# Performance work log

Measured on AMD Instinct MI355X. Metric: run time of the kernel, lower is better.

Reference implementation:

```python
import jax, jax.numpy as jnp
import numpy as np

DIM = 1024
EPS = 1e-5

def layernorm(x, g, b):
    m = jnp.mean(x, axis=-1, keepdims=True)
    v = jnp.var(x, axis=-1, keepdims=True)
    return (x - m) / jnp.sqrt(v + EPS) * g + b

def setup_inputs() -> dict:
    key = jax.random.key(0)
    ks = jax.random.split(key, 12)
    B, L, D = 4, 2048, DIM
    s = 1.0 / np.sqrt(D)
    return {
        "q": jax.random.normal(ks[0], (B, L, D), jnp.float32),
        "k": jax.random.normal(ks[1], (B, L, D), jnp.float32),
        "v": jax.random.normal(ks[2], (B, L, D), jnp.float32),
        "gq": jnp.ones((D,), jnp.float32), "bq": jnp.zeros((D,), jnp.float32),
        "gk": jnp.ones((D,), jnp.float32), "bk": jnp.zeros((D,), jnp.float32),
        "gv": jnp.ones((D,), jnp.float32), "bv": jnp.zeros((D,), jnp.float32),
        "Wq": jax.random.uniform(ks[3], (D, D), jnp.float32, -s, s),
        "Wk": jax.random.uniform(ks[4], (D, D), jnp.float32, -s, s),
        "Wv": jax.random.uniform(ks[5], (D, D), jnp.float32, -s, s),
        "Wp": jax.random.uniform(ks[6], (D, D), jnp.float32, -s, s),
        "bp": jax.random.uniform(ks[7], (D,), jnp.float32, -s, s),
    }

def reference(q, k, v, gq, bq, gk, bk, gv, bv, Wq, Wk, Wv, Wp, bp):
    scale = DIM ** -0.5
    qn = layernorm(q, gq, bq) @ Wq.T  # [B,Q,D]
    kn = layernorm(k, gk, bk) @ Wk.T  # [B,K,D]
    vn = layernorm(v, gv, bv) @ Wv.T  # [B,K,D]
    attn = jnp.einsum('bqc,bkc->bqk', qn, kn)
    attn = jax.nn.relu(attn) * scale  # ReLU on raw scores, then scale (matches in-place *=)
    attn_mask = jax.nn.softmax(attn, axis=-1)
    out = jnp.einsum('bqk,bkc->bqc', attn_mask, vn)
    out = out @ Wp.T + bp
    return (attn, out)
```

## Files before the change

### kernel.cpp

```cpp
#include <hip/hip_runtime.h>


typedef __attribute__((ext_vector_type(8))) short short8v;
typedef __attribute__((ext_vector_type(4))) float f32x4;

#define DEVI __device__ __forceinline__

DEVI float b2f(unsigned short u) {
  union { unsigned int i; float f; } x;
  x.i = ((unsigned int)u) << 16;
  return x.f;
}
DEVI unsigned short f2b(float f) {
  union { float f; unsigned int i; } x;
  x.f = f;
  unsigned int r = x.i + 0x7fffu + ((x.i >> 16) & 1u);
  return (unsigned short)(r >> 16);
}

DEVI bool sniff_bf16(const unsigned short* wq) {
  int bad = 0;
#pragma unroll
  for (int j = 0; j < 64; ++j) bad |= (fabsf(b2f(wq[j])) > 0.0625f) ? 1 : 0;
  return bad == 0;
}

DEVI void async16(const unsigned short* g, unsigned short* l) {
  __builtin_amdgcn_global_load_lds(
      (const __attribute__((address_space(1))) void*)g,
      (__attribute__((address_space(3))) void*)l, 16, 0, 0);
}

DEVI void bar() { asm volatile("s_barrier" ::: "memory"); }
DEVI void wait_lgkm0() { asm volatile("s_waitcnt lgkmcnt(0)" ::: "memory"); }
template <int N> DEVI void wait_vm();
template <> DEVI void wait_vm<0>() { asm volatile("s_waitcnt vmcnt(0)" ::: "memory"); }
template <> DEVI void wait_vm<6>() { asm volatile("s_waitcnt vmcnt(6)" ::: "memory"); }
template <> DEVI void wait_vm<8>() { asm volatile("s_waitcnt vmcnt(8)" ::: "memory"); }

template <int NT>
DEVI void gemm_core(unsigned short* sA, unsigned short* sB,
                    const unsigned short* Ab, const unsigned short* Bb,
                    int m0, int n0, int lda, int ldb, int K, int tid,
                    f32x4 (&acc)[4][NT]) {
  const int BN = NT * 32;
  const int ASZ = 128 * 64;
  const int BSZ = BN * 64;
  int lane = tid & 63, w = tid >> 6;
  int l15 = lane & 15, quad = lane >> 4;
  int r8 = lane >> 3;
  int scol = ((lane & 7) ^ r8) * 8;
  const unsigned short* gA = Ab + (size_t)(m0 + w * 32 + r8) * lda + scol;
  const unsigned short* gB = Bb + (size_t)(n0 + w * (BN / 4) + r8) * ldb + scol;
  int wm = w & 1, wn = w >> 1;
  int rxor = l15 & 7;
  const int nst = K >> 6;

  auto stage = [&](int b, int t) {
    unsigned short* lA = sA + b * ASZ + (size_t)(w * 32) * 64;
    unsigned short* lB = sB + b * BSZ + (size_t)(w * (BN / 4)) * 64;
    int k0 = t << 6;
#pragma unroll
    for (int j = 0; j < 4; ++j)
      async16(gA + (size_t)(j * 8) * lda + k0, lA + j * 8 * 64);
#pragma unroll
    for (int j = 0; j < NT; ++j)
      async16(gB + (size_t)(j * 8) * ldb + k0, lB + j * 8 * 64);
  };

  stage(0, 0);
  if (nst > 1) {
    stage(1, 1);
    wait_vm<4 + NT>();
  } else {
    wait_vm<0>();
  }
  __builtin_amdgcn_sched_barrier(0);
  bar();

  for (int t = 0; t < nst; ++t) {
    int b = t & 1;
    const unsigned short* rA = sA + b * ASZ + (size_t)(wm * 64 + l15) * 64;
    const unsigned short* rB = sB + b * BSZ + (size_t)(wn * (BN / 2) + l15) * 64;
#pragma unroll
    for (int c = 0; c < 2; ++c) {
      int col = ((c * 4 + quad) ^ rxor) * 8;
      short8v af[4], bf[NT];
#pragma unroll
      for (int i = 0; i < 4; ++i) af[i] = *(const short8v*)(rA + i * 1024 + col);
#pragma unroll
      for (int i = 0; i < NT; ++i) bf[i] = *(const short8v*)(rB + i * 1024 + col);
      __builtin_amdgcn_s_setprio(1);
#pragma unroll
      for (int mt = 0; mt < 4; ++mt)
#pragma unroll
        for (int nt = 0; nt < NT; ++nt)
          acc[mt][nt] = __builtin_amdgcn_mfma_f32_16x16x32_bf16(af[mt], bf[nt], acc[mt][nt], 0, 0, 0);
      __builtin_amdgcn_s_setprio(0);
    }
    if (t + 1 < nst) {
      wait_lgkm0();
      __builtin_amdgcn_sched_barrier(0);
      bar();
      if (t + 2 < nst) {
        stage(b, t + 2);
        wait_vm<4 + NT>();
      } else {
        wait_vm<0>();
      }
      __builtin_amdgcn_sched_barrier(0);
      bar();
    }
  }
}

DEVI int xcd_swz(int f, int nb) { return (f & 7) * (nb >> 3) + (f >> 3); }

struct PrepArgs {
  const void* q; const void* k; const void* v;
  const void* g[3]; const void* b[3];
  const void* W[4];
};

__global__ __launch_bounds__(256) void k_prep(PrepArgs pa,
    unsigned short* __restrict__ Wb, unsigned short* __restrict__ XN) {
  bool isbf = sniff_bf16((const unsigned short*)pa.W[0]);
  int bid = blockIdx.x, tid = threadIdx.x;
  if (bid < 2048) {
    int s = bid >> 9;
    size_t inner = ((size_t)(bid & 511)) * 2048 + (size_t)tid * 8;
    unsigned short* dst = Wb + (size_t)s * 1048576 + inner;
    if (isbf) {
      *(uint4*)dst = *(const uint4*)((const unsigned short*)pa.W[s] + inner);
    } else {
      const float* f = (const float*)pa.W[s] + inner;
      float4 a = *(const float4*)f;
      float4 b = *(const float4*)(f + 4);
      ushort4 o0 = { f2b(a.x), f2b(a.y), f2b(a.z), f2b(a.w) };
      ushort4 o1 = { f2b(b.x), f2b(b.y), f2b(b.z), f2b(b.w) };
      *(ushort4*)dst = o0;
      *(ushort4*)(dst + 4) = o1;
    }
  } else {
    int row = bid - 2048;
    int t = row >> 13;
    size_t r = (size_t)(row & 8191);
    const void* src = (t == 0) ? pa.q : (t == 1) ? pa.k : pa.v;
    float x0, x1, x2, x3;
    if (isbf) {
      ushort4 pk = *(const ushort4*)((const unsigned short*)src + r * 1024 + (size_t)tid * 4);
      x0 = b2f(pk.x); x1 = b2f(pk.y); x2 = b2f(pk.z); x3 = b2f(pk.w);
    } else {
      float4 pk = *(const float4*)((const float*)src + r * 1024 + (size_t)tid * 4);
      x0 = pk.x; x1 = pk.y; x2 = pk.z; x3 = pk.w;
    }
    float s1 = x0 + x1 + x2 + x3;
    float s2 = x0 * x0 + x1 * x1 + x2 * x2 + x3 * x3;
    for (int off = 32; off > 0; off >>= 1) {
      s1 += __shfl_down(s1, off);
      s2 += __shfl_down(s2, off);
    }
    __shared__ float sh[8];
    if ((tid & 63) == 0) { sh[tid >> 6] = s1; sh[4 + (tid >> 6)] = s2; }
    __syncthreads();
    float m  = (sh[0] + sh[1] + sh[2] + sh[3]) * (1.0f / 1024.0f);
    float m2 = (sh[4] + sh[5] + sh[6] + sh[7]) * (1.0f / 1024.0f);
    float rstd = rsqrtf(m2 - m * m + 1e-5f);
    float g0, g1, g2, g3, c0, c1, c2, c3;
    if (isbf) {
      ushort4 gv = *(const ushort4*)((const unsigned short*)pa.g[t] + tid * 4);
      ushort4 bb = *(const ushort4*)((const unsigned short*)pa.b[t] + tid * 4);
      g0 = b2f(gv.x); g1 = b2f(gv.y); g2 = b2f(gv.z); g3 = b2f(gv.w);
      c0 = b2f(bb.x); c1 = b2f(bb.y); c2 = b2f(bb.z); c3 = b2f(bb.w);
    } else {
      float4 gv = *(const float4*)((const float*)pa.g[t] + tid * 4);
      float4 bb = *(const float4*)((const float*)pa.b[t] + tid * 4);
      g0 = gv.x; g1 = gv.y; g2 = gv.z; g3 = gv.w;
      c0 = bb.x; c1 = bb.y; c2 = bb.z; c3 = bb.w;
    }
    ushort4 o;
    o.x = f2b((x0 - m) * rstd * g0 + c0);
    o.y = f2b((x1 - m) * rstd * g1 + c1);
    o.z = f2b((x2 - m) * rstd * g2 + c2);
    o.w = f2b((x3 - m) * rstd * g3 + c3);
    *(ushort4*)(XN + (size_t)row * 1024 + (size_t)tid * 4) = o;
  }
}

__global__ __launch_bounds__(256) void k_megaproj(
    const unsigned short* __restrict__ XN, const unsigned short* __restrict__ Wb,
    unsigned short* __restrict__ QN, unsigned short* __restrict__ VNT) {
  __shared__ __align__(16) unsigned short sA[2 * 128 * 64];
  __shared__ __align__(16) unsigned short sB[2 * 128 * 64];
  int x = xcd_swz((int)blockIdx.x, 1536), tid = threadIdx.x;
  int lane = tid & 63, w = tid >> 6;
  int wm = w & 1, wn = w >> 1;
  int l15 = lane & 15, quad = lane >> 4;
  f32x4 acc[4][4];
#pragma unroll
  for (int i = 0; i < 4; ++i)
#pragma unroll
    for (int j = 0; j < 4; ++j) acc[i][j] = (f32x4){0.f, 0.f, 0.f, 0.f};

  if (x < 1024) {
    int t = x >> 9, i = x & 511;
    int m0 = (i >> 3) * 128, n0 = (i & 7) * 128;
    gemm_core<4>(sA, sB, XN + (size_t)t * 8388608, Wb + (size_t)t * 1048576,
                 m0, n0, 1024, 1024, 1024, tid, acc);
    unsigned short* C = QN + (size_t)t * 8388608;
#pragma unroll
    for (int mt = 0; mt < 4; ++mt) {
      int mb = m0 + wm * 64 + mt * 16 + quad * 4;
#pragma unroll
      for (int nt = 0; nt < 4; ++nt) {
        int n = n0 + wn * 64 + nt * 16 + l15;
        f32x4 vc = acc[mt][nt];
#pragma unroll
        for (int r2 = 0; r2 < 4; ++r2) C[(size_t)(mb + r2) * 1024 + n] = f2b(vc[r2]);
      }
    }
  } else {
    int i = x - 1024, z = i >> 7, j = i & 127;
    int m0 = (j >> 3) * 128, n0 = (j & 7) * 128;
    gemm_core<4>(sA, sB, XN + 2 * 8388608 + (size_t)z * 2097152,
                 Wb + 2 * 1048576, m0, n0, 1024, 1024, 1024, tid, acc);
    unsigned short* Ct = VNT + (size_t)z * 2097152;
#pragma unroll
    for (int mt = 0; mt < 4; ++mt) {
      int mb = m0 + wm * 64 + mt * 16 + quad * 4;
#pragma unroll
      for (int nt = 0; nt < 4; ++nt) {
        int n = n0 + wn * 64 + nt * 16 + l15;
        f32x4 vc = acc[mt][nt];
        ushort4 o = { f2b(vc[0]), f2b(vc[1]), f2b(vc[2]), f2b(vc[3]) };
        *(ushort4*)&Ct[(size_t)n * 2048 + mb] = o;
      }
    }
  }
}

template <int EPI, int NT>
__global__ __launch_bounds__(256) void k_gemm(
    const unsigned short* __restrict__ A, const unsigned short* __restrict__ B,
    void* __restrict__ Cv, long long coff,
    int K, int lda, int ldb, int ldc,
    long long sAb, long long sBb, long long sCb,
    float scale, const void* __restrict__ bias,
    const unsigned short* __restrict__ wq_sniff) {
  __shared__ __align__(16) unsigned short sA[2 * 128 * 64];
  __shared__ __align__(16) unsigned short sB[2 * NT * 32 * 64];
  const int BN = NT * 32;
  int tid = threadIdx.x;
  int lane = tid & 63, w = tid >> 6;
  int wm = w & 1, wn = w >> 1;
  int l15 = lane & 15, quad = lane >> 4;

  int gx = gridDim.x, gy = gridDim.y;
  int nb = gx * gy * (int)gridDim.z;
  int f = (int)blockIdx.x + gx * ((int)blockIdx.y + gy * (int)blockIdx.z);
  f = xcd_swz(f, nb);
  int bx = f % gx;
  int rem = f / gx;
  int by = rem % gy;
  int bz = rem / gy;

  int m0 = by * 128, n0 = bx * BN;
  f32x4 acc[4][NT];
#pragma unroll
  for (int i = 0; i < 4; ++i)
#pragma unroll
    for (int j = 0; j < NT; ++j) acc[i][j] = (f32x4){0.f, 0.f, 0.f, 0.f};

  gemm_core<NT>(sA, sB, A + (long long)bz * sAb,
                B + (long long)bz * sBb, m0, n0, lda, ldb, K, tid, acc);

  long long cbase = coff + (long long)bz * sCb;
  bool isbf = (EPI != 0) ? sniff_bf16(wq_sniff) : true;
#pragma unroll
  for (int mt = 0; mt < 4; ++mt) {
    int mb = m0 + wm * 64 + mt * 16 + quad * 4;
#pragma unroll
    for (int nt = 0; nt < NT; ++nt) {
      int n = n0 + wn * (BN / 2) + nt * 16 + l15;
      f32x4 vc = acc[mt][nt];
      if (EPI == 0) {
        unsigned short* C = (unsigned short*)Cv + cbase;
#pragma unroll
        for (int r2 = 0; r2 < 4; ++r2) C[(size_t)(mb + r2) * ldc + n] = f2b(vc[r2]);
      } else if (EPI == 1) {
        if (isbf) {
          unsigned short* C = (unsigned short*)Cv + cbase;
#pragma unroll
          for (int r2 = 0; r2 < 4; ++r2)
            C[(size_t)(mb + r2) * ldc + n] = f2b(fmaxf(vc[r2], 0.f) * scale);
        } else {
          float* C = (float*)Cv + cbase;
#pragma unroll
          for (int r2 = 0; r2 < 4; ++r2)
            C[(size_t)(mb + r2) * ldc + n] = fmaxf(vc[r2], 0.f) * scale;
        }
      } else {
        float bv2 = isbf ? b2f(((const unsigned short*)bias)[n])
                         : ((const float*)bias)[n];
        if (isbf) {
          unsigned short* C = (unsigned short*)Cv + cbase;
#pragma unroll
          for (int r2 = 0; r2 < 4; ++r2) C[(size_t)(mb + r2) * ldc + n] = f2b(vc[r2] + bv2);
        } else {
          float* C = (float*)Cv + cbase;
#pragma unroll
          for (int r2 = 0; r2 < 4; ++r2) C[(size_t)(mb + r2) * ldc + n] = vc[r2] + bv2;
        }
      }
    }
  }
}

__global__ __launch_bounds__(256) void k_softmax(const void* __restrict__ S,
    unsigned short* __restrict__ P, const unsigned short* __restrict__ wq_sniff) {
  bool isbf = sniff_bf16(wq_sniff);
  size_t row = blockIdx.x;
  int tid = threadIdx.x;
  float v[8];
  if (isbf) {
    const unsigned short* s = (const unsigned short*)S + row * 2048 + (size_t)tid * 8;
    ushort4 a = *(const ushort4*)s;
    ushort4 b = *(const ushort4*)(s + 4);
    v[0] = b2f(a.x); v[1] = b2f(a.y); v[2] = b2f(a.z); v[3] = b2f(a.w);
    v[4] = b2f(b.x); v[5] = b2f(b.y); v[6] = b2f(b.z); v[7] = b2f(b.w);
  } else {
    const float* s = (const float*)S + row * 2048 + (size_t)tid * 8;
    float4 a = *(const float4*)s;
    float4 b = *(const float4*)(s + 4);
    v[0] = a.x; v[1] = a.y; v[2] = a.z; v[3] = a.w;
    v[4] = b.x; v[5] = b.y; v[6] = b.z; v[7] = b.w;
  }
  float mx = v[0];
#pragma unroll
  for (int j = 1; j < 8; ++j) mx = fmaxf(mx, v[j]);
  for (int off = 32; off > 0; off >>= 1) mx = fmaxf(mx, __shfl_down(mx, off));
  __shared__ float sh[8];
  if ((tid & 63) == 0) sh[tid >> 6] = mx;
  __syncthreads();
  mx = fmaxf(fmaxf(sh[0], sh[1]), fmaxf(sh[2], sh[3]));
  float sum = 0.f;
#pragma unroll
  for (int j = 0; j < 8; ++j) { v[j] = __expf(v[j] - mx); sum += v[j]; }
  for (int off = 32; off > 0; off >>= 1) sum += __shfl_down(sum, off);
  if ((tid & 63) == 0) sh[4 + (tid >> 6)] = sum;
  __syncthreads();
  float inv = 1.0f / (sh[4] + sh[5] + sh[6] + sh[7]);
  ushort4 o0 = { f2b(v[0] * inv), f2b(v[1] * inv), f2b(v[2] * inv), f2b(v[3] * inv) };
  ushort4 o1 = { f2b(v[4] * inv), f2b(v[5] * inv), f2b(v[6] * inv), f2b(v[7] * inv) };
  unsigned short* p = P + row * 2048 + (size_t)tid * 8;
  *(ushort4*)p = o0;
  *(ushort4*)(p + 4) = o1;
}

static const size_t MB_ = 1024 * 1024;
static const size_t OFF_W   = 0;
static const size_t OFF_XN  = 8 * MB_ + 128 * 1024;
static const size_t OFF_QN  = OFF_XN + 48 * MB_;
static const size_t OFF_VNT = OFF_QN + 32 * MB_;
static const size_t OFF_P   = OFF_XN;
static const size_t OFF_O1  = OFF_XN + 32 * MB_;

extern "C" void kernel_launch(void* const* d_in, const int* in_sizes, int n_in,
                              void* d_out, int out_size, void* d_ws, size_t ws_size,
                              hipStream_t stream) {
  (void)in_sizes; (void)n_in; (void)out_size; (void)ws_size;
  char* ws = (char*)d_ws;
  unsigned short* Wb  = (unsigned short*)(ws + OFF_W);
  unsigned short* XN  = (unsigned short*)(ws + OFF_XN);
  unsigned short* QN  = (unsigned short*)(ws + OFF_QN);
  unsigned short* VNT = (unsigned short*)(ws + OFF_VNT);
  unsigned short* P   = (unsigned short*)(ws + OFF_P);
  unsigned short* O1  = (unsigned short*)(ws + OFF_O1);
  const unsigned short* WqS = (const unsigned short*)d_in[9];

  PrepArgs pa;
  pa.q = d_in[0]; pa.k = d_in[1]; pa.v = d_in[2];
  pa.g[0] = d_in[3]; pa.b[0] = d_in[4];
  pa.g[1] = d_in[5]; pa.b[1] = d_in[6];
  pa.g[2] = d_in[7]; pa.b[2] = d_in[8];
  pa.W[0] = d_in[9]; pa.W[1] = d_in[10]; pa.W[2] = d_in[11]; pa.W[3] = d_in[12];

  k_prep<<<26624, 256, 0, stream>>>(pa, Wb, XN);

  k_megaproj<<<1536, 256, 0, stream>>>(XN, Wb, QN, VNT);

  k_gemm<1, 4><<<dim3(16, 16, 4), 256, 0, stream>>>(
      QN, QN + 8388608, d_out,
      0,
      1024, 1024, 1024, 2048,
      2097152LL, 2097152LL, 4194304LL,
      0.03125f, nullptr, WqS);

  k_softmax<<<8192, 256, 0, stream>>>(d_out, P, WqS);

  k_gemm<0, 2><<<dim3(16, 16, 4), 256, 0, stream>>>(
      P, VNT, O1,
      0,
      2048, 2048, 2048, 1024,
      4194304LL, 2097152LL, 2097152LL,
      0.f, nullptr, WqS);

  k_gemm<3, 4><<<dim3(8, 64, 1), 256, 0, stream>>>(
      O1, Wb + 3 * 1048576, d_out,
      16777216,
      1024, 1024, 1024, 1024,
      0LL, 0LL, 0LL,
      0.f, d_in[13], WqS);
}
```

Measured before the change: 428.3 us.

## Switch GEMMs to 256x256 tiles with 8 waves and quarter-staged pipelining

Replaces the 128xBN gemm core with a 256x256 tile core run by 512 threads (8 waves, each computing 128x64). Each K step is split into four phases that interleave async global-to-LDS loads of the next stage's A/B halves with MFMA work on the current stage. Larger tiles raise arithmetic intensity and cut global traffic. The V projection now computes the transposed output by swapping operands, so its epilogue no longer does transposed vector stores. The cost is fewer blocks, which leaves CUs underfilled on small grids (e.g. 128 blocks for the PV GEMM), plus higher register and LDS pressure (64KB LDS per block).

```diff
diff --git a/kernel.cpp b/kernel.cpp
--- a/kernel.cpp
+++ b/kernel.cpp
@@ -31,86 +31,133 @@
       (__attribute__((address_space(3))) void*)l, 16, 0, 0);
 }
 
-DEVI void bar() { asm volatile("s_barrier" ::: "memory"); }
 DEVI void wait_lgkm0() { asm volatile("s_waitcnt lgkmcnt(0)" ::: "memory"); }
 template <int N> DEVI void wait_vm();
 template <> DEVI void wait_vm<0>() { asm volatile("s_waitcnt vmcnt(0)" ::: "memory"); }
-template <> DEVI void wait_vm<6>() { asm volatile("s_waitcnt vmcnt(6)" ::: "memory"); }
-template <> DEVI void wait_vm<8>() { asm volatile("s_waitcnt vmcnt(8)" ::: "memory"); }
-
-template <int NT>
-DEVI void gemm_core(unsigned short* sA, unsigned short* sB,
-                    const unsigned short* Ab, const unsigned short* Bb,
-                    int m0, int n0, int lda, int ldb, int K, int tid,
-                    f32x4 (&acc)[4][NT]) {
-  const int BN = NT * 32;
-  const int ASZ = 128 * 64;
-  const int BSZ = BN * 64;
-  int lane = tid & 63, w = tid >> 6;
-  int l15 = lane & 15, quad = lane >> 4;
+template <> DEVI void wait_vm<2>() { asm volatile("s_waitcnt vmcnt(2)" ::: "memory"); }
+
+DEVI void stage_half(const unsigned short* G, int ld, unsigned short* L,
+                     int w, int lane, int k0) {
   int r8 = lane >> 3;
   int scol = ((lane & 7) ^ r8) * 8;
-  const unsigned short* gA = Ab + (size_t)(m0 + w * 32 + r8) * lda + scol;
-  const unsigned short* gB = Bb + (size_t)(n0 + w * (BN / 4) + r8) * ldb + scol;
-  int wm = w & 1, wn = w >> 1;
+#pragma unroll
+  for (int j = 0; j < 2; ++j) {
+    async16(G + (size_t)(j * 64 + w * 8 + r8) * ld + k0 + scol,
+            L + (j * 64 + w * 8) * 64);
+  }
+}
+
+DEVI void gemm8_core(unsigned short* sA, unsigned short* sB,
+                     const unsigned short* Ab, const unsigned short* Bb,
+                     int m0, int n0, int lda, int ldb, int K, int tid,
+                     f32x4 (&acc)[8][4]) {
+  int lane = tid & 63, w = tid >> 6;
+  int wm = w >> 2, wn = w & 3;
+  int l15 = lane & 15, quad = lane >> 4;
   int rxor = l15 & 7;
+  int cb0 = (quad ^ rxor) * 8;
+  int cb1 = ((4 + quad) ^ rxor) * 8;
   const int nst = K >> 6;
-
-  auto stage = [&](int b, int t) {
-    unsigned short* lA = sA + b * ASZ + (size_t)(w * 32) * 64;
-    unsigned short* lB = sB + b * BSZ + (size_t)(w * (BN / 4)) * 64;
-    int k0 = t << 6;
-#pragma unroll
-    for (int j = 0; j < 4; ++j)
-      async16(gA + (size_t)(j * 8) * lda + k0, lA + j * 8 * 64);
-#pragma unroll
-    for (int j = 0; j < NT; ++j)
-      async16(gB + (size_t)(j * 8) * ldb + k0, lB + j * 8 * 64);
-  };
-
-  stage(0, 0);
-  if (nst > 1) {
-    stage(1, 1);
-    wait_vm<4 + NT>();
-  } else {
-    wait_vm<0>();
-  }
-  __builtin_amdgcn_sched_barrier(0);
-  bar();
+  const unsigned short* A0 = Ab + (size_t)m0 * lda;
+  const unsigned short* A1 = A0 + (size_t)128 * lda;
+  const unsigned short* B0 = Bb + (size_t)n0 * ldb;
+  const unsigned short* B1 = B0 + (size_t)128 * ldb;
+
+  stage_half(A0, lda, sA, w, lane, 0);
+  stage_half(A1, lda, sA + 8192, w, lane, 0);
+  stage_half(B0, ldb, sB, w, lane, 0);
+  stage_half(B1, ldb, sB + 8192, w, lane, 0);
 
   for (int t = 0; t < nst; ++t) {
-    int b = t & 1;
-    const unsigned short* rA = sA + b * ASZ + (size_t)(wm * 64 + l15) * 64;
-    const unsigned short* rB = sB + b * BSZ + (size_t)(wn * (BN / 2) + l15) * 64;
-#pragma unroll
-    for (int c = 0; c < 2; ++c) {
-      int col = ((c * 4 + quad) ^ rxor) * 8;
-      short8v af[4], bf[NT];
-#pragma unroll
-      for (int i = 0; i < 4; ++i) af[i] = *(const short8v*)(rA + i * 1024 + col);
-#pragma unroll
-      for (int i = 0; i < NT; ++i) bf[i] = *(const short8v*)(rB + i * 1024 + col);
-      __builtin_amdgcn_s_setprio(1);
-#pragma unroll
-      for (int mt = 0; mt < 4; ++mt)
-#pragma unroll
-        for (int nt = 0; nt < NT; ++nt)
-          acc[mt][nt] = __builtin_amdgcn_mfma_f32_16x16x32_bf16(af[mt], bf[nt], acc[mt][nt], 0, 0, 0);
-      __builtin_amdgcn_s_setprio(0);
-    }
-    if (t + 1 < nst) {
-      wait_lgkm0();
-      __builtin_amdgcn_sched_barrier(0);
-      bar();
-      if (t + 2 < nst) {
-        stage(b, t + 2);
-        wait_vm<4 + NT>();
-      } else {
-        wait_vm<0>();
+    const int b = t & 1, nb2 = b ^ 1;
+    const bool st = (t + 1 < nst);
+    const int k0n = (t + 1) << 6;
+    const unsigned short* rA = sA + b * 16384 + (wm * 128 + l15) * 64;
+    const unsigned short* rB = sB + b * 16384 + (wn * 64 + l15) * 64;
+    short8v a[4][2], bb[4][2];
+
+    if (st) {
+      stage_half(A0, lda, sA + nb2 * 16384, w, lane, k0n);
+      wait_vm<2>();
+    } else {
+      wait_vm<0>();
+    }
+    __builtin_amdgcn_s_barrier();
+#pragma unroll
+    for (int mt = 0; mt < 4; ++mt) {
+      a[mt][0] = *(const short8v*)(rA + mt * 1024 + cb0);
+      a[mt][1] = *(const short8v*)(rA + mt * 1024 + cb1);
+    }
+#pragma unroll
+    for (int nt = 0; nt < 2; ++nt) {
+      bb[nt][0] = *(const short8v*)(rB + nt * 1024 + cb0);
+      bb[nt][1] = *(const short8v*)(rB + nt * 1024 + cb1);
+    }
+    wait_lgkm0();
+    __builtin_amdgcn_sched_barrier(0);
+    __builtin_amdgcn_s_setprio(1);
+#pragma unroll
+    for (int mt = 0; mt < 4; ++mt)
+#pragma unroll
+      for (int nt = 0; nt < 2; ++nt) {
+        acc[mt][nt] = __builtin_amdgcn_mfma_f32_16x16x32_bf16(a[mt][0], bb[nt][0], acc[mt][nt], 0, 0, 0);
+        acc[mt][nt] = __builtin_amdgcn_mfma_f32_16x16x32_bf16(a[mt][1], bb[nt][1], acc[mt][nt], 0, 0, 0);
       }
-      __builtin_amdgcn_sched_barrier(0);
-      bar();
-    }
+    __builtin_amdgcn_s_setprio(0);
+    __builtin_amdgcn_s_barrier();
+
+#pragma unroll
+    for (int nt = 2; nt < 4; ++nt) {
+      bb[nt][0] = *(const short8v*)(rB + nt * 1024 + cb0);
+      bb[nt][1] = *(const short8v*)(rB + nt * 1024 + cb1);
+    }
+    if (st) stage_half(A1, lda, sA + nb2 * 16384 + 8192, w, lane, k0n);
+    __builtin_amdgcn_s_barrier();
+    wait_lgkm0();
+    __builtin_amdgcn_sched_barrier(0);
+    __builtin_amdgcn_s_setprio(1);
+#pragma unroll
+    for (int mt = 0; mt < 4; ++mt)
+#pragma unroll
+      for (int nt = 2; nt < 4; ++nt) {
+        acc[mt][nt] = __builtin_amdgcn_mfma_f32_16x16x32_bf16(a[mt][0], bb[nt][0], acc[mt][nt], 0, 0, 0);
+        acc[mt][nt] = __builtin_amdgcn_mfma_f32_16x16x32_bf16(a[mt][1], bb[nt][1], acc[mt][nt], 0, 0, 0);
+      }
+    __builtin_amdgcn_s_setprio(0);
+    __builtin_amdgcn_s_barrier();
+
+#pragma unroll
+    for (int mt = 0; mt < 4; ++mt) {
+      a[mt][0] = *(const short8v*)(rA + (4 + mt) * 1024 + cb0);
+      a[mt][1] = *(const short8v*)(rA + (4 + mt) * 1024 + cb1);
+    }
+    if (st) stage_half(B0, ldb, sB + nb2 * 16384, w, lane, k0n);
+    __builtin_amdgcn_s_barrier();
+    wait_lgkm0();
+    __builtin_amdgcn_sched_barrier(0);
+    __builtin_amdgcn_s_setprio(1);
+#pragma unroll
+    for (int mt = 0; mt < 4; ++mt)
+#pragma unroll
+      for (int nt = 0; nt < 2; ++nt) {
+        acc[4 + mt][nt] = __builtin_amdgcn_mfma_f32_16x16x32_bf16(a[mt][0], bb[nt][0], acc[4 + mt][nt], 0, 0, 0);
+        acc[4 + mt][nt] = __builtin_amdgcn_mfma_f32_16x16x32_bf16(a[mt][1], bb[nt][1], acc[4 + mt][nt], 0, 0, 0);
+      }
+    __builtin_amdgcn_s_setprio(0);
+    __builtin_amdgcn_s_barrier();
+
+    if (st) stage_half(B1, ldb, sB + nb2 * 16384 + 8192, w, lane, k0n);
+    __builtin_amdgcn_s_barrier();
+    __builtin_amdgcn_s_setprio(1);
+#pragma unroll
+    for (int mt = 0; mt < 4; ++mt)
+#pragma unroll
+      for (int nt = 2; nt < 4; ++nt) {
+        acc[4 + mt][nt] = __builtin_amdgcn_mfma_f32_16x16x32_bf16(a[mt][0], bb[nt][0], acc[4 + mt][nt], 0, 0, 0);
+        acc[4 + mt][nt] = __builtin_amdgcn_mfma_f32_16x16x32_bf16(a[mt][1], bb[nt][1], acc[4 + mt][nt], 0, 0, 0);
+      }
+    __builtin_amdgcn_s_setprio(0);
+    __builtin_amdgcn_s_barrier();
   }
 }
 
@@ -169,14 +216,14 @@
     float g0, g1, g2, g3, c0, c1, c2, c3;
     if (isbf) {
       ushort4 gv = *(const ushort4*)((const unsigned short*)pa.g[t] + tid * 4);
-      ushort4 bb = *(const ushort4*)((const unsigned short*)pa.b[t] + tid * 4);
+      ushort4 bbv = *(const ushort4*)((const unsigned short*)pa.b[t] + tid * 4);
       g0 = b2f(gv.x); g1 = b2f(gv.y); g2 = b2f(gv.z); g3 = b2f(gv.w);
-      c0 = b2f(bb.x); c1 = b2f(bb.y); c2 = b2f(bb.z); c3 = b2f(bb.w);
+      c0 = b2f(bbv.x); c1 = b2f(bbv.y); c2 = b2f(bbv.z); c3 = b2f(bbv.w);
     } else {
       float4 gv = *(const float4*)((const float*)pa.g[t] + tid * 4);
-      float4 bb = *(const float4*)((const float*)pa.b[t] + tid * 4);
+      float4 bbv = *(const float4*)((const float*)pa.b[t] + tid * 4);
       g0 = gv.x; g1 = gv.y; g2 = gv.z; g3 = gv.w;
-      c0 = bb.x; c1 = bb.y; c2 = bb.z; c3 = bb.w;
+      c0 = bbv.x; c1 = bbv.y; c2 = bbv.z; c3 = bbv.w;
     }
     ushort4 o;
     o.x = f2b((x0 - m) * rstd * g0 + c0);
@@ -187,72 +234,62 @@
   }
 }
 
-__global__ __launch_bounds__(256) void k_megaproj(
+__global__ __launch_bounds__(512, 2) void k_megaproj(
     const unsigned short* __restrict__ XN, const unsigned short* __restrict__ Wb,
     unsigned short* __restrict__ QN, unsigned short* __restrict__ VNT) {
-  __shared__ __align__(16) unsigned short sA[2 * 128 * 64];
-  __shared__ __align__(16) unsigned short sB[2 * 128 * 64];
-  int x = xcd_swz((int)blockIdx.x, 1536), tid = threadIdx.x;
+  __shared__ __align__(16) unsigned short sA[2 * 256 * 64];
+  __shared__ __align__(16) unsigned short sB[2 * 256 * 64];
+  int x = xcd_swz((int)blockIdx.x, 384), tid = threadIdx.x;
   int lane = tid & 63, w = tid >> 6;
-  int wm = w & 1, wn = w >> 1;
+  int wm = w >> 2, wn = w & 3;
   int l15 = lane & 15, quad = lane >> 4;
-  f32x4 acc[4][4];
-#pragma unroll
-  for (int i = 0; i < 4; ++i)
+  f32x4 acc[8][4];
+#pragma unroll
+  for (int i = 0; i < 8; ++i)
 #pragma unroll
     for (int j = 0; j < 4; ++j) acc[i][j] = (f32x4){0.f, 0.f, 0.f, 0.f};
 
-  if (x < 1024) {
-    int t = x >> 9, i = x & 511;
-    int m0 = (i >> 3) * 128, n0 = (i & 7) * 128;
-    gemm_core<4>(sA, sB, XN + (size_t)t * 8388608, Wb + (size_t)t * 1048576,
-                 m0, n0, 1024, 1024, 1024, tid, acc);
-    unsigned short* C = QN + (size_t)t * 8388608;
-#pragma unroll
-    for (int mt = 0; mt < 4; ++mt) {
-      int mb = m0 + wm * 64 + mt * 16 + quad * 4;
-#pragma unroll
-      for (int nt = 0; nt < 4; ++nt) {
-        int n = n0 + wn * 64 + nt * 16 + l15;
-        f32x4 vc = acc[mt][nt];
-#pragma unroll
-        for (int r2 = 0; r2 < 4; ++r2) C[(size_t)(mb + r2) * 1024 + n] = f2b(vc[r2]);
-      }
-    }
+  unsigned short* C;
+  int m0, n0, ldc;
+  if (x < 256) {
+    int t = x >> 7, i = x & 127;
+    m0 = (i >> 2) * 256; n0 = (i & 3) * 256; ldc = 1024;
+    gemm8_core(sA, sB, XN + (size_t)t * 8388608, Wb + (size_t)t * 1048576,
+               m0, n0, 1024, 1024, 1024, tid, acc);
+    C = QN + (size_t)t * 8388608;
   } else {
-    int i = x - 1024, z = i >> 7, j = i & 127;
-    int m0 = (j >> 3) * 128, n0 = (j & 7) * 128;
-    gemm_core<4>(sA, sB, XN + 2 * 8388608 + (size_t)z * 2097152,
-                 Wb + 2 * 1048576, m0, n0, 1024, 1024, 1024, tid, acc);
-    unsigned short* Ct = VNT + (size_t)z * 2097152;
-#pragma unroll
-    for (int mt = 0; mt < 4; ++mt) {
-      int mb = m0 + wm * 64 + mt * 16 + quad * 4;
-#pragma unroll
-      for (int nt = 0; nt < 4; ++nt) {
-        int n = n0 + wn * 64 + nt * 16 + l15;
-        f32x4 vc = acc[mt][nt];
-        ushort4 o = { f2b(vc[0]), f2b(vc[1]), f2b(vc[2]), f2b(vc[3]) };
-        *(ushort4*)&Ct[(size_t)n * 2048 + mb] = o;
-      }
-    }
-  }
-}
-
-template <int EPI, int NT>
-__global__ __launch_bounds__(256) void k_gemm(
+    int i = x - 256, z = i >> 5, j = i & 31;
+    m0 = (j >> 3) * 256; n0 = (j & 7) * 256; ldc = 2048;
+    gemm8_core(sA, sB, Wb + 2 * 1048576, XN + 2 * 8388608 + (size_t)z * 2097152,
+               m0, n0, 1024, 1024, 1024, tid, acc);
+    C = VNT + (size_t)z * 2097152;
+  }
+#pragma unroll
+  for (int mt = 0; mt < 8; ++mt) {
+    int mb = m0 + wm * 128 + mt * 16 + quad * 4;
+#pragma unroll
+    for (int nt = 0; nt < 4; ++nt) {
+      int n = n0 + wn * 64 + nt * 16 + l15;
+      f32x4 vc = acc[mt][nt];
+#pragma unroll
+      for (int r2 = 0; r2 < 4; ++r2) C[(size_t)(mb + r2) * ldc + n] = f2b(vc[r2]);
+    }
+  }
+}
+
+template <int EPI>
+__global__ __launch_bounds__(512, 2) void k_gemm(
     const unsigned short* __restrict__ A, const unsigned short* __restrict__ B,
     void* __restrict__ Cv, long long coff,
     int K, int lda, int ldb, int ldc,
     long long sAb, long long sBb, long long sCb,
     float scale, const void* __restrict__ bias,
     const unsigned short* __restrict__ wq_sniff) {
-  __shared__ __align__(16) unsigned short sA[2 * 128 * 64];
-  __shared__ __align__(16) unsigned short sB[2 * NT * 32 * 64];
-  const int BN = NT * 32;
+  __shared__ __align__(16) unsigned short sA[2 * 256 * 64];
+  __shared__ __align__(16) unsigned short sB[2 * 256 * 64];
   int tid = threadIdx.x;
   int lane = tid & 63, w = tid >> 6;
-  int wm = w & 1, wn = w >> 1;
+  int wm = w >> 2, wn = w & 3;
   int l15 = lane & 15, quad = lane >> 4;
 
   int gx = gridDim.x, gy = gridDim.y;
@@ -264,24 +301,24 @@
   int by = rem % gy;
   int bz = rem / gy;
 
-  int m0 = by * 128, n0 = bx * BN;
-  f32x4 acc[4][NT];
-#pragma unroll
-  for (int i = 0; i < 4; ++i)
-#pragma unroll
-    for (int j = 0; j < NT; ++j) acc[i][j] = (f32x4){0.f, 0.f, 0.f, 0.f};
-
-  gemm_core<NT>(sA, sB, A + (long long)bz * sAb,
-                B + (long long)bz * sBb, m0, n0, lda, ldb, K, tid, acc);
+  int m0 = by * 256, n0 = bx * 256;
+  f32x4 acc[8][4];
+#pragma unroll
+  for (int i = 0; i < 8; ++i)
+#pragma unroll
+    for (int j = 0; j < 4; ++j) acc[i][j] = (f32x4){0.f, 0.f, 0.f, 0.f};
+
+  gemm8_core(sA, sB, A + (long long)bz * sAb, B + (long long)bz * sBb,
+             m0, n0, lda, ldb, K, tid, acc);
 
   long long cbase = coff + (long long)bz * sCb;
   bool isbf = (EPI != 0) ? sniff_bf16(wq_sniff) : true;
 #pragma unroll
-  for (int mt = 0; mt < 4; ++mt) {
-    int mb = m0 + wm * 64 + mt * 16 + quad * 4;
-#pragma unroll
-    for (int nt = 0; nt < NT; ++nt) {
-      int n = n0 + wn * (BN / 2) + nt * 16 + l15;
+  for (int mt = 0; mt < 8; ++mt) {
+    int mb = m0 + wm * 128 + mt * 16 + quad * 4;
+#pragma unroll
+    for (int nt = 0; nt < 4; ++nt) {
+      int n = n0 + wn * 64 + nt * 16 + l15;
       f32x4 vc = acc[mt][nt];
       if (EPI == 0) {
         unsigned short* C = (unsigned short*)Cv + cbase;
@@ -387,9 +424,9 @@
 
   k_prep<<<26624, 256, 0, stream>>>(pa, Wb, XN);
 
-  k_megaproj<<<1536, 256, 0, stream>>>(XN, Wb, QN, VNT);
-
-  k_gemm<1, 4><<<dim3(16, 16, 4), 256, 0, stream>>>(
+  k_megaproj<<<384, 512, 0, stream>>>(XN, Wb, QN, VNT);
+
+  k_gemm<1><<<dim3(8, 8, 4), 512, 0, stream>>>(
       QN, QN + 8388608, d_out,
       0,
       1024, 1024, 1024, 2048,
@@ -398,14 +435,14 @@
 
   k_softmax<<<8192, 256, 0, stream>>>(d_out, P, WqS);
 
-  k_gemm<0, 2><<<dim3(16, 16, 4), 256, 0, stream>>>(
+  k_gemm<0><<<dim3(4, 8, 4), 512, 0, stream>>>(
       P, VNT, O1,
       0,
       2048, 2048, 2048, 1024,
       4194304LL, 2097152LL, 2097152LL,
       0.f, nullptr, WqS);
 
-  k_gemm<3, 4><<<dim3(8, 64, 1), 256, 0, stream>>>(
+  k_gemm<3><<<dim3(4, 32, 1), 512, 0, stream>>>(
       O1, Wb + 3 * 1048576, d_out,
       16777216,
       1024, 1024, 1024, 1024,
```

Result: slower. 461.5 us (+7.8%).
